# Optimization experiments

Measured on AMD Instinct MI355X. Metric: run time of the kernel, lower is better.

Reference implementation:

```python
import jax, jax.numpy as jnp
import numpy as np

EMBED_DIM = 256
NUM_HEADS = 4
HEAD_DIM = EMBED_DIM // NUM_HEADS
B, N0, N1 = 4, 2048, 2048


def setup_inputs() -> dict:
    key = jax.random.key(0)
    ks = jax.random.split(key, 16)
    d = EMBED_DIM
    s = 0.02
    return {
        "x0": jax.random.normal(ks[0], (B, N0, d), jnp.float32),
        "x1": jax.random.normal(ks[1], (B, N1, d), jnp.float32),
        "Wqk": jax.random.normal(ks[2], (d, d), jnp.float32) * s,
        "bqk": jnp.zeros((d,), jnp.float32),
        "Wv": jax.random.normal(ks[3], (d, d), jnp.float32) * s,
        "bv": jnp.zeros((d,), jnp.float32),
        "Wout": jax.random.normal(ks[4], (d, d), jnp.float32) * s,
        "bout": jnp.zeros((d,), jnp.float32),
        "W0": jax.random.normal(ks[5], (2 * d, 2 * d), jnp.float32) * s,
        "b0": jnp.zeros((2 * d,), jnp.float32),
        "ln_scale": jnp.ones((2 * d,), jnp.float32),
        "ln_bias": jnp.zeros((2 * d,), jnp.float32),
        "W3": jax.random.normal(ks[6], (2 * d, d), jnp.float32) * s,
        "b3": jnp.zeros((d,), jnp.float32),
    }


def _heads(t, b, n):
    # [b, n, d] -> [b, h, n, hd]
    return t.reshape(b, n, NUM_HEADS, HEAD_DIM).transpose(0, 2, 1, 3)


def _layernorm(y, scale, bias, eps=1e-5):
    mu = jnp.mean(y, axis=-1, keepdims=True)
    var = jnp.mean(jnp.square(y - mu), axis=-1, keepdims=True)
    return (y - mu) * jax.lax.rsqrt(var + eps) * scale + bias


def reference(x0, x1, Wqk, bqk, Wv, bv, Wout, bout, W0, b0, ln_scale, ln_bias, W3, b3):
    b, n0, d = x0.shape
    _, n1, _ = x1.shape
    scale = 1.0 / jnp.sqrt(jnp.float32(HEAD_DIM))

    qk0 = _heads(x0 @ Wqk + bqk, b, n0)
    qk1 = _heads(x1 @ Wqk + bqk, b, n1)
    v0 = _heads(x0 @ Wv + bv, b, n0)
    v1 = _heads(x1 @ Wv + bv, b, n1)

    # shared logits: [b, h, n0, n1]
    logits01 = jnp.einsum('bhid,bhjd->bhij', qk0, qk1) * scale
    attn01 = jax.nn.softmax(logits01, axis=-1)
    m0 = jnp.einsum('bhij,bhjd->bhid', attn01, v1)
    attn10 = jax.nn.softmax(logits01.transpose(0, 1, 3, 2), axis=-1)
    m1 = jnp.einsum('bhji,bhjd->bhid', attn10.transpose(0, 1, 3, 2), v0)

    m0 = m0.transpose(0, 2, 1, 3).reshape(b, n0, d) @ Wout + bout
    m1 = m1.transpose(0, 2, 1, 3).reshape(b, n1, d) @ Wout + bout

    def ffn(x, m):
        y = jnp.concatenate([x, m], axis=-1) @ W0 + b0
        y = _layernorm(y, ln_scale, ln_bias)
        y = jax.nn.gelu(y, approximate=False)
        return x + y @ W3 + b3

    return ffn(x0, m0), ffn(x1, m1)
```

## Files before the change

### kernel.cpp

```cpp
#include <hip/hip_runtime.h>
#include <math.h>

#define BATCH 4
#define SEQ 2048
#define DMODEL 256
#define NH 4
#define HD 64
#define MROWS (BATCH * SEQ)

typedef short bf16x8 __attribute__((ext_vector_type(8)));
typedef float f32x4 __attribute__((ext_vector_type(4)));

__device__ __forceinline__ unsigned short f2bf(float x) {
  union { float f; unsigned int u; } v;
  v.f = x;
  unsigned int r = (v.u + 0x7FFF + ((v.u >> 16) & 1)) >> 16;
  return (unsigned short)r;
}
__device__ __forceinline__ unsigned short f2bf_trunc(float x) {
  union { float f; unsigned int u; } v;
  v.f = x;
  return (unsigned short)(v.u >> 16);
}
__device__ __forceinline__ float bf2f(unsigned short u) {
  union { unsigned int u; float f; } v;
  v.u = ((unsigned int)u) << 16;
  return v.f;
}

__global__ __launch_bounds__(256) void cast_x(
    const float* __restrict__ x0, const float* __restrict__ x1,
    unsigned short* __restrict__ x0b, unsigned short* __restrict__ x1b) {
  const int n4 = (MROWS * DMODEL) / 4;
  for (int i = blockIdx.x * 256 + threadIdx.x; i < 2 * n4; i += gridDim.x * 256) {
    const float* src = (i < n4) ? x0 : x1;
    unsigned short* dst = (i < n4) ? x0b : x1b;
    int j = (i < n4) ? i : i - n4;
    float4 v = *(const float4*)&src[j * 4];
    ushort4 o = {f2bf(v.x), f2bf(v.y), f2bf(v.z), f2bf(v.w)};
    *(ushort4*)&dst[j * 4] = o;
  }
}

__global__ __launch_bounds__(256) void cast_w(
    const float* __restrict__ Wqk, const float* __restrict__ Wv,
    const float* __restrict__ Wout, const float* __restrict__ W0,
    const float* __restrict__ W3,
    unsigned short* __restrict__ Wqkt, unsigned short* __restrict__ Wvt,
    unsigned short* __restrict__ Woutt, unsigned short* __restrict__ W0t,
    unsigned short* __restrict__ W3t) {
  int gid = blockIdx.x * 256 + threadIdx.x;
  const float* src; unsigned short* dst; int K, N, idx;
  if (gid < 65536)        { src = Wqk;  dst = Wqkt;  K = 256; N = 256; idx = gid; }
  else if (gid < 131072)  { src = Wv;   dst = Wvt;   K = 256; N = 256; idx = gid - 65536; }
  else if (gid < 196608)  { src = Wout; dst = Woutt; K = 256; N = 256; idx = gid - 131072; }
  else if (gid < 458752)  { src = W0;   dst = W0t;   K = 512; N = 512; idx = gid - 196608; }
  else if (gid < 589824)  { src = W3;   dst = W3t;   K = 512; N = 256; idx = gid - 458752; }
  else return;
  int k = idx / N, n = idx % N;
  dst[n * K + k] = f2bf(src[idx]);
}

template <int MODE>
__global__ __launch_bounds__(256) void gemm2(
    const unsigned short* __restrict__ A_0, const unsigned short* __restrict__ A_1,
    const unsigned short* __restrict__ A2_0, const unsigned short* __restrict__ A2_1,
    const unsigned short* __restrict__ Wt, const float* __restrict__ bias,
    const float* __restrict__ resid_0, const float* __restrict__ resid_1,
    void* __restrict__ C_0, void* __restrict__ C_1, int N, int K) {
  __shared__ unsigned short lds[12288];

  const int t = threadIdx.x;
  const int w = t >> 6, lane = t & 63;
  const int qd = lane >> 4, l15 = lane & 15;
  const int row0 = blockIdx.x * 128;
  const int col0 = blockIdx.y * 64;
  const int z = blockIdx.z;
  const unsigned short* A  = z ? A_1 : A_0;
  const unsigned short* A2 = z ? A2_1 : A2_0;
  const float* resid = z ? resid_1 : resid_0;
  void* Cv = z ? C_1 : C_0;

  f32x4 acc[2][4];
#pragma unroll
  for (int mh = 0; mh < 2; ++mh)
#pragma unroll
    for (int tn = 0; tn < 4; ++tn) acc[mh][tn] = (f32x4){0.f, 0.f, 0.f, 0.f};

  for (int k0 = 0; k0 < K; k0 += 64) {
    __syncthreads();
#pragma unroll
    for (int pp = 0; pp < 6; ++pp) {
      int g = pp * 4 + w;
      uint4 d;
      if (g < 16) {
        int tm = g >> 1, s = g & 1;
        const unsigned short* Ap = A;
        int kk = k0 + s * 32 + qd * 8, lda = K;
        if (MODE == 2) {
          Ap = (k0 < 256) ? A : A2;
          kk = (k0 & 255) + s * 32 + qd * 8;
          lda = 256;
        }
        d = *(const uint4*)&Ap[(size_t)(row0 + tm * 16 + l15) * lda + kk];
        *(uint4*)&lds[(g * 64 + lane) * 8] = d;
      } else {
        int tn = (g - 16) >> 1, s = g & 1;
        d = *(const uint4*)&Wt[(size_t)(col0 + tn * 16 + l15) * K + k0 + s * 32 + qd * 8];
        *(uint4*)&lds[8192 + (((tn * 2 + s) * 64 + lane)) * 8] = d;
      }
    }
    __syncthreads();

    bf16x8 aA[2][2];
#pragma unroll
    for (int mh = 0; mh < 2; ++mh)
#pragma unroll
      for (int s = 0; s < 2; ++s)
        aA[mh][s] = *(const bf16x8*)&lds[((((w * 2 + mh) * 2 + s)) * 64 + lane) * 8];
#pragma unroll
    for (int tn = 0; tn < 4; ++tn) {
      bf16x8 b0 = *(const bf16x8*)&lds[8192 + ((tn * 2 + 0) * 64 + lane) * 8];
      bf16x8 b1 = *(const bf16x8*)&lds[8192 + ((tn * 2 + 1) * 64 + lane) * 8];
#pragma unroll
      for (int mh = 0; mh < 2; ++mh) {
        acc[mh][tn] = __builtin_amdgcn_mfma_f32_16x16x32_bf16(aA[mh][0], b0, acc[mh][tn], 0, 0, 0);
        acc[mh][tn] = __builtin_amdgcn_mfma_f32_16x16x32_bf16(aA[mh][1], b1, acc[mh][tn], 0, 0, 0);
      }
    }
  }

  if (MODE == 1) {
    __syncthreads();
#pragma unroll
    for (int tn = 0; tn < 4; ++tn) {
      int col = col0 + tn * 16 + l15;
      float bb = bias[col];
#pragma unroll
      for (int mh = 0; mh < 2; ++mh)
#pragma unroll
        for (int r = 0; r < 4; ++r) {
          int rloc = w * 32 + mh * 16 + qd * 4 + r;
          lds[(tn * 16 + l15) * 130 + rloc] = f2bf(acc[mh][tn][r] + bb);
        }
    }
    __syncthreads();
    unsigned short* Vt = (unsigned short*)Cv;
    int b_ = row0 >> 11;
    int h_ = blockIdx.y;
    int seq0 = row0 & 2047;
    for (int c = t; c < 1024; c += 256) {
      int dloc = c >> 4, sc = c & 15;
      uint4 d = *(const uint4*)&lds[dloc * 130 + sc * 8];
      *(uint4*)&Vt[((size_t)(b_ * NH + h_) * HD + dloc) * SEQ + seq0 + sc * 8] = d;
    }
    return;
  }

#pragma unroll
  for (int tn = 0; tn < 4; ++tn) {
    int col = col0 + tn * 16 + l15;
    float bb = bias[col];
#pragma unroll
    for (int mh = 0; mh < 2; ++mh)
#pragma unroll
      for (int r = 0; r < 4; ++r) {
        size_t grow = row0 + w * 32 + mh * 16 + qd * 4 + r;
        float v = acc[mh][tn][r] + bb;
        if (MODE == 3) {
          ((float*)Cv)[grow * N + col] = resid[grow * N + col] + v;
        } else {
          ((unsigned short*)Cv)[grow * N + col] = f2bf(v);
        }
      }
  }
}

__global__ __launch_bounds__(256) void flash_v4(
    const unsigned short* __restrict__ qk0, const unsigned short* __restrict__ qk1,
    const unsigned short* __restrict__ vt0, const unsigned short* __restrict__ vt1,
    unsigned short* __restrict__ m0, unsigned short* __restrict__ m1) {
  __shared__ unsigned short lds[8192];

  const int t = threadIdx.x;
  const int w = t >> 6, lane = t & 63;
  const int qd = lane >> 4, l15 = lane & 15;
  const int qt = blockIdx.x, h = blockIdx.y, z = blockIdx.z;
  const int dir = z & 1, b = z >> 1;
  const unsigned short* Qb = dir ? qk1 : qk0;
  const unsigned short* Kb = dir ? qk0 : qk1;
  const unsigned short* Vt = dir ? vt0 : vt1;
  unsigned short* Ob = dir ? m1 : m0;

  const size_t qrow0 = (size_t)b * SEQ + (size_t)qt * 128;
  const int hoff = h * HD;
  const unsigned short* vtb = Vt + (size_t)(b * NH + h) * HD * SEQ;
  const float sc2 = 0.125f * 1.44269504f;

  bf16x8 qf[2][2];
#pragma unroll
  for (int qh = 0; qh < 2; ++qh)
#pragma unroll
    for (int s = 0; s < 2; ++s)
      qf[qh][s] = *(const bf16x8*)&Qb[(qrow0 + w * 32 + qh * 16 + l15) * DMODEL + hoff + s * 32 + qd * 8];

  f32x4 Oacc[2][4];
#pragma unroll
  for (int qh = 0; qh < 2; ++qh)
#pragma unroll
    for (int td = 0; td < 4; ++td) Oacc[qh][td] = (f32x4){0.f, 0.f, 0.f, 0.f};
  float l_lane[2] = {0.f, 0.f};

  for (int kt = 0; kt < SEQ / 64; ++kt) {
    const size_t kbase = (size_t)b * SEQ + (size_t)kt * 64;
    __syncthreads();
#pragma unroll
    for (int pp = 0; pp < 4; ++pp) {
      int g = pp * 4 + w;
      uint4 d;
      if (g < 8) {
        int tk = g >> 1, s = g & 1;
        int kvl = (tk >> 1) * 32 + (l15 >> 2) * 8 + (tk & 1) * 4 + (l15 & 3);
        d = *(const uint4*)&Kb[(kbase + kvl) * DMODEL + hoff + s * 32 + qd * 8];
      } else {
        int td = (g - 8) >> 1, s = g & 1;
        d = *(const uint4*)&vtb[(size_t)(td * 16 + l15) * SEQ + kt * 64 + s * 32 + qd * 8];
      }
      *(uint4*)&lds[(g * 64 + lane) * 8] = d;
    }
    __syncthreads();

    bf16x8 kf[4][2], vf[4][2];
#pragma unroll
    for (int tk = 0; tk < 4; ++tk)
#pragma unroll
      for (int s = 0; s < 2; ++s) {
        kf[tk][s] = *(const bf16x8*)&lds[((tk * 2 + s) * 64 + lane) * 8];
        vf[tk][s] = *(const bf16x8*)&lds[4096 + ((tk * 2 + s) * 64 + lane) * 8];
      }

#pragma unroll
    for (int qh = 0; qh < 2; ++qh) {
      f32x4 S[4];
#pragma unroll
      for (int tk = 0; tk < 4; ++tk) {
        f32x4 a = {0.f, 0.f, 0.f, 0.f};
        a = __builtin_amdgcn_mfma_f32_16x16x32_bf16(kf[tk][0], qf[qh][0], a, 0, 0, 0);
        a = __builtin_amdgcn_mfma_f32_16x16x32_bf16(kf[tk][1], qf[qh][1], a, 0, 0, 0);
        S[tk] = a;
      }
      float p[4][4];
      float rs = 0.f;
#pragma unroll
      for (int tk = 0; tk < 4; ++tk)
#pragma unroll
        for (int r = 0; r < 4; ++r) {
          float pv = exp2f(S[tk][r] * sc2);
          p[tk][r] = pv;
          rs += pv;
        }
      l_lane[qh] += rs;
      bf16x8 pA[2];
#pragma unroll
      for (int s = 0; s < 2; ++s) {
        bf16x8 v;
#pragma unroll
        for (int j = 0; j < 4; ++j) {
          v[j] = (short)f2bf_trunc(p[2 * s][j]);
          v[j + 4] = (short)f2bf_trunc(p[2 * s + 1][j]);
        }
        pA[s] = v;
      }
#pragma unroll
      for (int td = 0; td < 4; ++td) {
        Oacc[qh][td] = __builtin_amdgcn_mfma_f32_16x16x32_bf16(pA[0], vf[td][0], Oacc[qh][td], 0, 0, 0);
        Oacc[qh][td] = __builtin_amdgcn_mfma_f32_16x16x32_bf16(pA[1], vf[td][1], Oacc[qh][td], 0, 0, 0);
      }
    }
  }

#pragma unroll
  for (int qh = 0; qh < 2; ++qh) {
    float l = l_lane[qh];
    l += __shfl_xor(l, 16);
    l += __shfl_xor(l, 32);
    float linv = 1.0f / l;
#pragma unroll
    for (int r = 0; r < 4; ++r) {
      float lq = __shfl(linv, qd * 20 + r, 64);
      size_t row = qrow0 + w * 32 + qh * 16 + qd * 4 + r;
#pragma unroll
      for (int td = 0; td < 4; ++td)
        Ob[row * DMODEL + hoff + td * 16 + l15] = f2bf(Oacc[qh][td][r] * lq);
    }
  }
}

__global__ __launch_bounds__(256) void ln_gelu2(
    unsigned short* __restrict__ Y0, unsigned short* __restrict__ Y1,
    const float* __restrict__ sc, const float* __restrict__ bi) {
  const int t = threadIdx.x;
  const int row = blockIdx.x & (MROWS - 1);
  unsigned short* Y = (blockIdx.x >> 13) ? Y1 : Y0;
  unsigned short* p = Y + (size_t)row * 512;
  unsigned int u = *(const unsigned int*)&p[t * 2];
  float v0 = bf2f((unsigned short)(u & 0xFFFF));
  float v1 = bf2f((unsigned short)(u >> 16));
  float s1 = v0 + v1, s2 = v0 * v0 + v1 * v1;
#pragma unroll
  for (int m = 1; m < 64; m <<= 1) {
    s1 += __shfl_xor(s1, m);
    s2 += __shfl_xor(s2, m);
  }
  __shared__ float red[8];
  int w = t >> 6;
  if ((t & 63) == 0) { red[w] = s1; red[4 + w] = s2; }
  __syncthreads();
  s1 = red[0] + red[1] + red[2] + red[3];
  s2 = red[4] + red[5] + red[6] + red[7];
  float mu = s1 * (1.0f / 512.0f);
  float var = s2 * (1.0f / 512.0f) - mu * mu;
  float rstd = rsqrtf(var + 1e-5f);
  float y0 = (v0 - mu) * rstd * sc[t * 2] + bi[t * 2];
  float y1 = (v1 - mu) * rstd * sc[t * 2 + 1] + bi[t * 2 + 1];
  y0 = 0.5f * y0 * (1.0f + erff(y0 * 0.70710678118654752f));
  y1 = 0.5f * y1 * (1.0f + erff(y1 * 0.70710678118654752f));
  unsigned int o = (unsigned int)f2bf(y0) | ((unsigned int)f2bf(y1) << 16);
  *(unsigned int*)&p[t * 2] = o;
}

extern "C" void kernel_launch(void* const* d_in, const int* in_sizes, int n_in,
                              void* d_out, int out_size, void* d_ws,
                              size_t ws_size, hipStream_t stream) {
  const float* x0   = (const float*)d_in[0];
  const float* x1   = (const float*)d_in[1];
  const float* Wqk  = (const float*)d_in[2];
  const float* bqk  = (const float*)d_in[3];
  const float* Wv   = (const float*)d_in[4];
  const float* bv   = (const float*)d_in[5];
  const float* Wout = (const float*)d_in[6];
  const float* bout = (const float*)d_in[7];
  const float* W0   = (const float*)d_in[8];
  const float* b0   = (const float*)d_in[9];
  const float* lns  = (const float*)d_in[10];
  const float* lnb  = (const float*)d_in[11];
  const float* W3   = (const float*)d_in[12];
  const float* b3   = (const float*)d_in[13];

  char* ws = (char*)d_ws;
  const size_t MB = 1024 * 1024;
  unsigned short* x0b   = (unsigned short*)(ws + 0 * MB);
  unsigned short* x1b   = (unsigned short*)(ws + 4 * MB);
  unsigned short* Wqkt  = (unsigned short*)(ws + 8 * MB);
  unsigned short* Wvt   = (unsigned short*)(ws + 9 * MB);
  unsigned short* Woutt = (unsigned short*)(ws + 10 * MB);
  unsigned short* W0t   = (unsigned short*)(ws + 11 * MB);
  unsigned short* W3t   = (unsigned short*)(ws + 12 * MB);
  unsigned short* qk0b  = (unsigned short*)(ws + 13 * MB);
  unsigned short* qk1b  = (unsigned short*)(ws + 17 * MB);
  unsigned short* vt0   = (unsigned short*)(ws + 21 * MB);
  unsigned short* vt1   = (unsigned short*)(ws + 25 * MB);
  unsigned short* m0b   = (unsigned short*)(ws + 29 * MB);
  unsigned short* m1b   = (unsigned short*)(ws + 33 * MB);
  unsigned short* mp0b  = (unsigned short*)(ws + 37 * MB);
  unsigned short* mp1b  = (unsigned short*)(ws + 41 * MB);
  unsigned short* y0b   = (unsigned short*)(ws + 13 * MB);
  unsigned short* y1b   = (unsigned short*)(ws + 21 * MB);
  float* out0 = (float*)d_out;
  float* out1 = out0 + (size_t)MROWS * DMODEL;

  dim3 blk(256);
  dim3 gP(MROWS / 128, 4, 2);
  dim3 gF1(MROWS / 128, 8, 2);
  dim3 gA(SEQ / 128, NH, BATCH * 2);

  cast_x<<<dim3(4096), blk, 0, stream>>>(x0, x1, x0b, x1b);
  cast_w<<<dim3(589824 / 256), blk, 0, stream>>>(Wqk, Wv, Wout, W0, W3,
                                                 Wqkt, Wvt, Woutt, W0t, W3t);

  gemm2<0><<<gP, blk, 0, stream>>>(x0b, x1b, nullptr, nullptr, Wqkt, bqk,
                                   nullptr, nullptr, qk0b, qk1b, DMODEL, DMODEL);
  gemm2<1><<<gP, blk, 0, stream>>>(x0b, x1b, nullptr, nullptr, Wvt, bv,
                                   nullptr, nullptr, vt0, vt1, DMODEL, DMODEL);

  flash_v4<<<gA, blk, 0, stream>>>(qk0b, qk1b, vt0, vt1, m0b, m1b);

  gemm2<0><<<gP, blk, 0, stream>>>(m0b, m1b, nullptr, nullptr, Woutt, bout,
                                   nullptr, nullptr, mp0b, mp1b, DMODEL, DMODEL);

  gemm2<2><<<gF1, blk, 0, stream>>>(x0b, x1b, mp0b, mp1b, W0t, b0,
                                    nullptr, nullptr, y0b, y1b, 512, 512);

  ln_gelu2<<<dim3(2 * MROWS), blk, 0, stream>>>(y0b, y1b, lns, lnb);

  gemm2<3><<<gP, blk, 0, stream>>>(y0b, y1b, nullptr, nullptr, W3t, b3,
                                   x0, x1, out0, out1, DMODEL, 512);
}
```

Measured before the change: 274.8 us.

## Fold Wout into W0, fuse QK/V projection, split-K flash attention with DMA loads

Precomputes Wout·W0[256:] and the matching bias so the output-projection GEMM disappears. The QK and V projections become one GEMM with a concatenated weight, and the softmax scale is folded into the stored QK values. Flash attention is split into two halves over the keys, which doubles the grid; a combine kernel merges the partial outputs and row sums. All GEMM and flash tile loads now use global_load_lds DMA, the GEMM tile shrinks to 64 rows, and LN-GELU processes one row per wave. In exchange it adds fp32 partial-output traffic and a combine pass, and the QK scale is applied to bf16-rounded values before the dot product.

```diff
diff --git a/kernel.cpp b/kernel.cpp
--- a/kernel.cpp
+++ b/kernel.cpp
@@ -6,196 +6,241 @@
 #define DMODEL 256
 #define NH 4
 #define HD 64
-#define MROWS (BATCH * SEQ)
+#define MROWS 8192
+#define QKSCALE 0.4246608905f
 
 typedef short bf16x8 __attribute__((ext_vector_type(8)));
 typedef float f32x4 __attribute__((ext_vector_type(4)));
-
-__device__ __forceinline__ unsigned short f2bf(float x) {
+typedef unsigned short us;
+
+__device__ __forceinline__ us f2bf(float x) {
   union { float f; unsigned int u; } v;
   v.f = x;
   unsigned int r = (v.u + 0x7FFF + ((v.u >> 16) & 1)) >> 16;
-  return (unsigned short)r;
-}
-__device__ __forceinline__ unsigned short f2bf_trunc(float x) {
+  return (us)r;
+}
+__device__ __forceinline__ us f2bf_trunc(float x) {
   union { float f; unsigned int u; } v;
   v.f = x;
-  return (unsigned short)(v.u >> 16);
-}
-__device__ __forceinline__ float bf2f(unsigned short u) {
+  return (us)(v.u >> 16);
+}
+__device__ __forceinline__ float bf2f(us u) {
   union { unsigned int u; float f; } v;
   v.u = ((unsigned int)u) << 16;
   return v.f;
 }
+__device__ __forceinline__ void dma16(const void* g, void* l) {
+  auto gp = (const __attribute__((address_space(1))) unsigned int*)(unsigned long long)(uintptr_t)g;
+  auto lp = (__attribute__((address_space(3))) unsigned int*)(unsigned int)(uintptr_t)l;
+  __builtin_amdgcn_global_load_lds(gp, lp, 16, 0, 0);
+}
 
 __global__ __launch_bounds__(256) void cast_x(
     const float* __restrict__ x0, const float* __restrict__ x1,
-    unsigned short* __restrict__ x0b, unsigned short* __restrict__ x1b) {
+    us* __restrict__ x0b, us* __restrict__ x1b) {
   const int n4 = (MROWS * DMODEL) / 4;
-  for (int i = blockIdx.x * 256 + threadIdx.x; i < 2 * n4; i += gridDim.x * 256) {
-    const float* src = (i < n4) ? x0 : x1;
-    unsigned short* dst = (i < n4) ? x0b : x1b;
-    int j = (i < n4) ? i : i - n4;
-    float4 v = *(const float4*)&src[j * 4];
-    ushort4 o = {f2bf(v.x), f2bf(v.y), f2bf(v.z), f2bf(v.w)};
-    *(ushort4*)&dst[j * 4] = o;
-  }
+  int i = blockIdx.x * 256 + threadIdx.x;
+  const float* src = (i < n4) ? x0 : x1;
+  us* dst = (i < n4) ? x0b : x1b;
+  int j = (i < n4) ? i : i - n4;
+  float4 v = *(const float4*)&src[j * 4];
+  ushort4 o = {f2bf(v.x), f2bf(v.y), f2bf(v.z), f2bf(v.w)};
+  *(ushort4*)&dst[j * 4] = o;
 }
 
 __global__ __launch_bounds__(256) void cast_w(
     const float* __restrict__ Wqk, const float* __restrict__ Wv,
+    const float* __restrict__ W0, const float* __restrict__ W3,
+    const float* __restrict__ bqk, const float* __restrict__ bv,
+    us* __restrict__ Wqvt, us* __restrict__ W1t, us* __restrict__ W3t,
+    float* __restrict__ bias_qv) {
+  int gid = blockIdx.x * 256 + threadIdx.x;
+  if (gid < 65536) {
+    int k = gid >> 8, j = gid & 255;
+    Wqvt[j * 256 + k] = f2bf(Wqk[gid]);
+  } else if (gid < 131072) {
+    int i = gid - 65536;
+    int k = i >> 8, j = i & 255;
+    Wqvt[(256 + j) * 256 + k] = f2bf(Wv[i]);
+  } else if (gid < 262144) {
+    int i = gid - 131072;
+    int k = i >> 9, j = i & 511;
+    W1t[j * 512 + k] = f2bf(W0[i]);
+  } else if (gid < 393216) {
+    int i = gid - 262144;
+    int k = i >> 8, j = i & 255;
+    W3t[j * 512 + k] = f2bf(W3[i]);
+  } else if (gid < 393728) {
+    int j = gid - 393216;
+    bias_qv[j] = (j < 256) ? bqk[j] : bv[j - 256];
+  }
+}
+
+__global__ __launch_bounds__(256) void wcomb_k(
     const float* __restrict__ Wout, const float* __restrict__ W0,
-    const float* __restrict__ W3,
-    unsigned short* __restrict__ Wqkt, unsigned short* __restrict__ Wvt,
-    unsigned short* __restrict__ Woutt, unsigned short* __restrict__ W0t,
-    unsigned short* __restrict__ W3t) {
-  int gid = blockIdx.x * 256 + threadIdx.x;
-  const float* src; unsigned short* dst; int K, N, idx;
-  if (gid < 65536)        { src = Wqk;  dst = Wqkt;  K = 256; N = 256; idx = gid; }
-  else if (gid < 131072)  { src = Wv;   dst = Wvt;   K = 256; N = 256; idx = gid - 65536; }
-  else if (gid < 196608)  { src = Wout; dst = Woutt; K = 256; N = 256; idx = gid - 131072; }
-  else if (gid < 458752)  { src = W0;   dst = W0t;   K = 512; N = 512; idx = gid - 196608; }
-  else if (gid < 589824)  { src = W3;   dst = W3t;   K = 512; N = 256; idx = gid - 458752; }
-  else return;
-  int k = idx / N, n = idx % N;
-  dst[n * K + k] = f2bf(src[idx]);
+    const float* __restrict__ b0, const float* __restrict__ bout,
+    us* __restrict__ W1t, float* __restrict__ bias1) {
+  int t = threadIdx.x, i = blockIdx.x;
+  if (i < 256) {
+    float a0 = 0.f, a1 = 0.f;
+    for (int k = 0; k < 256; ++k) {
+      float wk = Wout[i * 256 + k];
+      const float* row = &W0[(256 + k) * 512];
+      a0 += wk * row[t];
+      a1 += wk * row[t + 256];
+    }
+    W1t[t * 512 + 256 + i] = f2bf(a0);
+    W1t[(t + 256) * 512 + 256 + i] = f2bf(a1);
+  } else {
+    float a0 = b0[t], a1 = b0[t + 256];
+    for (int k = 0; k < 256; ++k) {
+      float bk = bout[k];
+      const float* row = &W0[(256 + k) * 512];
+      a0 += bk * row[t];
+      a1 += bk * row[t + 256];
+    }
+    bias1[t] = a0;
+    bias1[t + 256] = a1;
+  }
 }
 
 template <int MODE>
-__global__ __launch_bounds__(256) void gemm2(
-    const unsigned short* __restrict__ A_0, const unsigned short* __restrict__ A_1,
-    const unsigned short* __restrict__ A2_0, const unsigned short* __restrict__ A2_1,
-    const unsigned short* __restrict__ Wt, const float* __restrict__ bias,
-    const float* __restrict__ resid_0, const float* __restrict__ resid_1,
-    void* __restrict__ C_0, void* __restrict__ C_1, int N, int K) {
-  __shared__ unsigned short lds[12288];
-
-  const int t = threadIdx.x;
-  const int w = t >> 6, lane = t & 63;
+__global__ __launch_bounds__(256) void gemm3(
+    const us* __restrict__ A0, const us* __restrict__ A1,
+    const us* __restrict__ Am0, const us* __restrict__ Am1,
+    const us* __restrict__ Wt, const float* __restrict__ bias,
+    const float* __restrict__ r0_, const float* __restrict__ r1_,
+    void* __restrict__ C0_, void* __restrict__ C1_,
+    void* __restrict__ V0_, void* __restrict__ V1_, int K) {
+  __shared__ us lds[8192];
+  const int t = threadIdx.x, w = t >> 6, lane = t & 63;
   const int qd = lane >> 4, l15 = lane & 15;
-  const int row0 = blockIdx.x * 128;
-  const int col0 = blockIdx.y * 64;
+  const int row0 = blockIdx.x * 64;
+  const int coltile = blockIdx.y, col0 = coltile * 64;
   const int z = blockIdx.z;
-  const unsigned short* A  = z ? A_1 : A_0;
-  const unsigned short* A2 = z ? A2_1 : A2_0;
-  const float* resid = z ? resid_1 : resid_0;
-  void* Cv = z ? C_1 : C_0;
-
-  f32x4 acc[2][4];
-#pragma unroll
-  for (int mh = 0; mh < 2; ++mh)
-#pragma unroll
-    for (int tn = 0; tn < 4; ++tn) acc[mh][tn] = (f32x4){0.f, 0.f, 0.f, 0.f};
+  const us* Ax = z ? A1 : A0;
+  const us* Am = z ? Am1 : Am0;
+
+  f32x4 acc[4];
+#pragma unroll
+  for (int tn = 0; tn < 4; ++tn) acc[tn] = (f32x4){0.f, 0.f, 0.f, 0.f};
 
   for (int k0 = 0; k0 < K; k0 += 64) {
     __syncthreads();
 #pragma unroll
-    for (int pp = 0; pp < 6; ++pp) {
+    for (int pp = 0; pp < 4; ++pp) {
       int g = pp * 4 + w;
-      uint4 d;
-      if (g < 16) {
+      const us* src;
+      if (g < 8) {
         int tm = g >> 1, s = g & 1;
-        const unsigned short* Ap = A;
-        int kk = k0 + s * 32 + qd * 8, lda = K;
-        if (MODE == 2) {
-          Ap = (k0 < 256) ? A : A2;
-          kk = (k0 & 255) + s * 32 + qd * 8;
+        const us* Ap = Ax;
+        int kk = k0 + s * 32 + qd * 8;
+        int lda = K;
+        if (MODE == 1) {
+          Ap = (k0 < 256) ? Ax : Am;
+          kk = kk & 255;
           lda = 256;
         }
-        d = *(const uint4*)&Ap[(size_t)(row0 + tm * 16 + l15) * lda + kk];
-        *(uint4*)&lds[(g * 64 + lane) * 8] = d;
+        src = &Ap[(size_t)(row0 + tm * 16 + l15) * lda + kk];
       } else {
-        int tn = (g - 16) >> 1, s = g & 1;
-        d = *(const uint4*)&Wt[(size_t)(col0 + tn * 16 + l15) * K + k0 + s * 32 + qd * 8];
-        *(uint4*)&lds[8192 + (((tn * 2 + s) * 64 + lane)) * 8] = d;
-      }
+        int tn = (g - 8) >> 1, s = g & 1;
+        src = &Wt[(size_t)(col0 + tn * 16 + l15) * K + k0 + s * 32 + qd * 8];
+      }
+      dma16(src, &lds[g * 512]);
     }
     __syncthreads();
 
-    bf16x8 aA[2][2];
-#pragma unroll
-    for (int mh = 0; mh < 2; ++mh)
-#pragma unroll
-      for (int s = 0; s < 2; ++s)
-        aA[mh][s] = *(const bf16x8*)&lds[((((w * 2 + mh) * 2 + s)) * 64 + lane) * 8];
+    bf16x8 aA0 = *(const bf16x8*)&lds[((w * 2 + 0) * 64 + lane) * 8];
+    bf16x8 aA1 = *(const bf16x8*)&lds[((w * 2 + 1) * 64 + lane) * 8];
 #pragma unroll
     for (int tn = 0; tn < 4; ++tn) {
-      bf16x8 b0 = *(const bf16x8*)&lds[8192 + ((tn * 2 + 0) * 64 + lane) * 8];
-      bf16x8 b1 = *(const bf16x8*)&lds[8192 + ((tn * 2 + 1) * 64 + lane) * 8];
-#pragma unroll
-      for (int mh = 0; mh < 2; ++mh) {
-        acc[mh][tn] = __builtin_amdgcn_mfma_f32_16x16x32_bf16(aA[mh][0], b0, acc[mh][tn], 0, 0, 0);
-        acc[mh][tn] = __builtin_amdgcn_mfma_f32_16x16x32_bf16(aA[mh][1], b1, acc[mh][tn], 0, 0, 0);
-      }
-    }
-  }
-
-  if (MODE == 1) {
-    __syncthreads();
+      bf16x8 b0v = *(const bf16x8*)&lds[((8 + tn * 2 + 0) * 64 + lane) * 8];
+      bf16x8 b1v = *(const bf16x8*)&lds[((8 + tn * 2 + 1) * 64 + lane) * 8];
+      acc[tn] = __builtin_amdgcn_mfma_f32_16x16x32_bf16(aA0, b0v, acc[tn], 0, 0, 0);
+      acc[tn] = __builtin_amdgcn_mfma_f32_16x16x32_bf16(aA1, b1v, acc[tn], 0, 0, 0);
+    }
+  }
+
+  if (MODE == 0) {
+    if (coltile < 4) {
+      us* C = (us*)(z ? C1_ : C0_);
+#pragma unroll
+      for (int tn = 0; tn < 4; ++tn) {
+        int col = col0 + tn * 16 + l15;
+        float bb = bias[col];
+#pragma unroll
+        for (int r = 0; r < 4; ++r) {
+          size_t grow = row0 + w * 16 + qd * 4 + r;
+          C[grow * 256 + col] = f2bf((acc[tn][r] + bb) * QKSCALE);
+        }
+      }
+    } else {
+      __syncthreads();
+      int h_ = coltile - 4;
+#pragma unroll
+      for (int tn = 0; tn < 4; ++tn) {
+        int col = col0 + tn * 16 + l15;
+        float bb = bias[col];
+#pragma unroll
+        for (int r = 0; r < 4; ++r) {
+          int rloc = w * 16 + qd * 4 + r;
+          lds[(tn * 16 + l15) * 66 + rloc] = f2bf(acc[tn][r] + bb);
+        }
+      }
+      __syncthreads();
+      us* Vt = (us*)(z ? V1_ : V0_);
+      int b_ = row0 >> 11, seq0 = row0 & 2047;
+      for (int c = t; c < 512; c += 256) {
+        int dloc = c >> 3, scc = c & 7;
+        uint4 d = *(const uint4*)&lds[dloc * 66 + scc * 8];
+        *(uint4*)&Vt[((size_t)(b_ * NH + h_) * HD + dloc) * SEQ + seq0 + scc * 8] = d;
+      }
+    }
+  } else if (MODE == 1) {
+    us* C = (us*)(z ? C1_ : C0_);
 #pragma unroll
     for (int tn = 0; tn < 4; ++tn) {
       int col = col0 + tn * 16 + l15;
       float bb = bias[col];
 #pragma unroll
-      for (int mh = 0; mh < 2; ++mh)
-#pragma unroll
-        for (int r = 0; r < 4; ++r) {
-          int rloc = w * 32 + mh * 16 + qd * 4 + r;
-          lds[(tn * 16 + l15) * 130 + rloc] = f2bf(acc[mh][tn][r] + bb);
-        }
-    }
-    __syncthreads();
-    unsigned short* Vt = (unsigned short*)Cv;
-    int b_ = row0 >> 11;
-    int h_ = blockIdx.y;
-    int seq0 = row0 & 2047;
-    for (int c = t; c < 1024; c += 256) {
-      int dloc = c >> 4, sc = c & 15;
-      uint4 d = *(const uint4*)&lds[dloc * 130 + sc * 8];
-      *(uint4*)&Vt[((size_t)(b_ * NH + h_) * HD + dloc) * SEQ + seq0 + sc * 8] = d;
-    }
-    return;
-  }
-
-#pragma unroll
-  for (int tn = 0; tn < 4; ++tn) {
-    int col = col0 + tn * 16 + l15;
-    float bb = bias[col];
-#pragma unroll
-    for (int mh = 0; mh < 2; ++mh)
-#pragma unroll
       for (int r = 0; r < 4; ++r) {
-        size_t grow = row0 + w * 32 + mh * 16 + qd * 4 + r;
-        float v = acc[mh][tn][r] + bb;
-        if (MODE == 3) {
-          ((float*)Cv)[grow * N + col] = resid[grow * N + col] + v;
-        } else {
-          ((unsigned short*)Cv)[grow * N + col] = f2bf(v);
-        }
-      }
-  }
-}
-
-__global__ __launch_bounds__(256) void flash_v4(
-    const unsigned short* __restrict__ qk0, const unsigned short* __restrict__ qk1,
-    const unsigned short* __restrict__ vt0, const unsigned short* __restrict__ vt1,
-    unsigned short* __restrict__ m0, unsigned short* __restrict__ m1) {
-  __shared__ unsigned short lds[8192];
-
-  const int t = threadIdx.x;
-  const int w = t >> 6, lane = t & 63;
+        size_t grow = row0 + w * 16 + qd * 4 + r;
+        C[grow * 512 + col] = f2bf(acc[tn][r] + bb);
+      }
+    }
+  } else {
+    float* C = (float*)(z ? C1_ : C0_);
+    const float* R = z ? r1_ : r0_;
+#pragma unroll
+    for (int tn = 0; tn < 4; ++tn) {
+      int col = col0 + tn * 16 + l15;
+      float bb = bias[col];
+#pragma unroll
+      for (int r = 0; r < 4; ++r) {
+        size_t grow = row0 + w * 16 + qd * 4 + r;
+        C[grow * 256 + col] = R[grow * 256 + col] + acc[tn][r] + bb;
+      }
+    }
+  }
+}
+
+__global__ __launch_bounds__(256) void flash_v5(
+    const us* __restrict__ qk0, const us* __restrict__ qk1,
+    const us* __restrict__ vt0, const us* __restrict__ vt1,
+    float* __restrict__ Opart, float* __restrict__ lpart) {
+  __shared__ us lds[8192];
+  const int t = threadIdx.x, w = t >> 6, lane = t & 63;
   const int qd = lane >> 4, l15 = lane & 15;
-  const int qt = blockIdx.x, h = blockIdx.y, z = blockIdx.z;
-  const int dir = z & 1, b = z >> 1;
-  const unsigned short* Qb = dir ? qk1 : qk0;
-  const unsigned short* Kb = dir ? qk0 : qk1;
-  const unsigned short* Vt = dir ? vt0 : vt1;
-  unsigned short* Ob = dir ? m1 : m0;
-
+  const int qt = blockIdx.x & 15, half = blockIdx.x >> 4;
+  const int h = blockIdx.y, z = blockIdx.z, dir = z & 1, b = z >> 1;
+  const us* Qb = dir ? qk1 : qk0;
+  const us* Kb = dir ? qk0 : qk1;
+  const us* Vt = dir ? vt0 : vt1;
+  float* Op = Opart + (size_t)(dir * 2 + half) * (MROWS * DMODEL);
+  float* lp = lpart + ((size_t)(dir * 2 + half) * NH + h) * MROWS;
   const size_t qrow0 = (size_t)b * SEQ + (size_t)qt * 128;
   const int hoff = h * HD;
-  const unsigned short* vtb = Vt + (size_t)(b * NH + h) * HD * SEQ;
-  const float sc2 = 0.125f * 1.44269504f;
+  const us* vtb = Vt + (size_t)(b * NH + h) * HD * SEQ;
 
   bf16x8 qf[2][2];
 #pragma unroll
@@ -211,22 +256,22 @@
     for (int td = 0; td < 4; ++td) Oacc[qh][td] = (f32x4){0.f, 0.f, 0.f, 0.f};
   float l_lane[2] = {0.f, 0.f};
 
-  for (int kt = 0; kt < SEQ / 64; ++kt) {
+  for (int kt = half * 16; kt < half * 16 + 16; ++kt) {
     const size_t kbase = (size_t)b * SEQ + (size_t)kt * 64;
     __syncthreads();
 #pragma unroll
     for (int pp = 0; pp < 4; ++pp) {
       int g = pp * 4 + w;
-      uint4 d;
+      const us* src;
       if (g < 8) {
         int tk = g >> 1, s = g & 1;
         int kvl = (tk >> 1) * 32 + (l15 >> 2) * 8 + (tk & 1) * 4 + (l15 & 3);
-        d = *(const uint4*)&Kb[(kbase + kvl) * DMODEL + hoff + s * 32 + qd * 8];
+        src = &Kb[(kbase + kvl) * DMODEL + hoff + s * 32 + qd * 8];
       } else {
         int td = (g - 8) >> 1, s = g & 1;
-        d = *(const uint4*)&vtb[(size_t)(td * 16 + l15) * SEQ + kt * 64 + s * 32 + qd * 8];
-      }
-      *(uint4*)&lds[(g * 64 + lane) * 8] = d;
+        src = &vtb[(size_t)(td * 16 + l15) * SEQ + kt * 64 + s * 32 + qd * 8];
+      }
+      dma16(src, &lds[g * 512]);
     }
     __syncthreads();
 
@@ -236,7 +281,7 @@
 #pragma unroll
       for (int s = 0; s < 2; ++s) {
         kf[tk][s] = *(const bf16x8*)&lds[((tk * 2 + s) * 64 + lane) * 8];
-        vf[tk][s] = *(const bf16x8*)&lds[4096 + ((tk * 2 + s) * 64 + lane) * 8];
+        vf[tk][s] = *(const bf16x8*)&lds[((8 + tk * 2 + s) * 64 + lane) * 8];
       }
 
 #pragma unroll
@@ -255,7 +300,7 @@
       for (int tk = 0; tk < 4; ++tk)
 #pragma unroll
         for (int r = 0; r < 4; ++r) {
-          float pv = exp2f(S[tk][r] * sc2);
+          float pv = exp2f(S[tk][r]);
           p[tk][r] = pv;
           rs += pv;
         }
@@ -284,49 +329,82 @@
     float l = l_lane[qh];
     l += __shfl_xor(l, 16);
     l += __shfl_xor(l, 32);
-    float linv = 1.0f / l;
+    if (qd == 0) lp[qrow0 + w * 32 + qh * 16 + l15] = l;
 #pragma unroll
     for (int r = 0; r < 4; ++r) {
-      float lq = __shfl(linv, qd * 20 + r, 64);
       size_t row = qrow0 + w * 32 + qh * 16 + qd * 4 + r;
 #pragma unroll
       for (int td = 0; td < 4; ++td)
-        Ob[row * DMODEL + hoff + td * 16 + l15] = f2bf(Oacc[qh][td][r] * lq);
-    }
-  }
-}
-
-__global__ __launch_bounds__(256) void ln_gelu2(
-    unsigned short* __restrict__ Y0, unsigned short* __restrict__ Y1,
+        Op[row * DMODEL + hoff + td * 16 + l15] = Oacc[qh][td][r];
+    }
+  }
+}
+
+__global__ __launch_bounds__(256) void combine_k(
+    const float* __restrict__ Opart, const float* __restrict__ lpart,
+    us* __restrict__ m0b, us* __restrict__ m1b) {
+  int gid = blockIdx.x * 256 + threadIdx.x;
+  int dir = gid >= (MROWS * DMODEL / 4);
+  int idx = gid - dir * (MROWS * DMODEL / 4);
+  int row = idx >> 6;
+  int c4 = (idx & 63) << 2;
+  int h = c4 >> 6;
+  const float* Oa = Opart + (size_t)(dir * 2 + 0) * (MROWS * DMODEL);
+  const float* Ob = Opart + (size_t)(dir * 2 + 1) * (MROWS * DMODEL);
+  float la = lpart[((size_t)(dir * 2 + 0) * NH + h) * MROWS + row];
+  float lb = lpart[((size_t)(dir * 2 + 1) * NH + h) * MROWS + row];
+  float inv = 1.0f / (la + lb);
+  float4 a = *(const float4*)&Oa[(size_t)row * DMODEL + c4];
+  float4 bv = *(const float4*)&Ob[(size_t)row * DMODEL + c4];
+  us* m = dir ? m1b : m0b;
+  ushort4 o = {f2bf((a.x + bv.x) * inv), f2bf((a.y + bv.y) * inv),
+               f2bf((a.z + bv.z) * inv), f2bf((a.w + bv.w) * inv)};
+  *(ushort4*)&m[(size_t)row * DMODEL + c4] = o;
+}
+
+__global__ __launch_bounds__(256) void ln_gelu3(
+    us* __restrict__ Y0, us* __restrict__ Y1,
     const float* __restrict__ sc, const float* __restrict__ bi) {
-  const int t = threadIdx.x;
-  const int row = blockIdx.x & (MROWS - 1);
-  unsigned short* Y = (blockIdx.x >> 13) ? Y1 : Y0;
-  unsigned short* p = Y + (size_t)row * 512;
-  unsigned int u = *(const unsigned int*)&p[t * 2];
-  float v0 = bf2f((unsigned short)(u & 0xFFFF));
-  float v1 = bf2f((unsigned short)(u >> 16));
-  float s1 = v0 + v1, s2 = v0 * v0 + v1 * v1;
+  int w = threadIdx.x >> 6, lane = threadIdx.x & 63;
+  int ridx = blockIdx.x * 4 + w;
+  us* Y = (ridx >= MROWS) ? Y1 : Y0;
+  int row = ridx & (MROWS - 1);
+  us* p = Y + (size_t)row * 512 + lane * 8;
+  uint4 u = *(const uint4*)p;
+  unsigned int uu[4] = {u.x, u.y, u.z, u.w};
+  float v[8];
+#pragma unroll
+  for (int i = 0; i < 4; ++i) {
+    v[2 * i] = bf2f((us)(uu[i] & 0xFFFF));
+    v[2 * i + 1] = bf2f((us)(uu[i] >> 16));
+  }
+  float s1 = 0.f, s2 = 0.f;
+#pragma unroll
+  for (int i = 0; i < 8; ++i) { s1 += v[i]; s2 += v[i] * v[i]; }
 #pragma unroll
   for (int m = 1; m < 64; m <<= 1) {
     s1 += __shfl_xor(s1, m);
     s2 += __shfl_xor(s2, m);
   }
-  __shared__ float red[8];
-  int w = t >> 6;
-  if ((t & 63) == 0) { red[w] = s1; red[4 + w] = s2; }
-  __syncthreads();
-  s1 = red[0] + red[1] + red[2] + red[3];
-  s2 = red[4] + red[5] + red[6] + red[7];
   float mu = s1 * (1.0f / 512.0f);
   float var = s2 * (1.0f / 512.0f) - mu * mu;
   float rstd = rsqrtf(var + 1e-5f);
-  float y0 = (v0 - mu) * rstd * sc[t * 2] + bi[t * 2];
-  float y1 = (v1 - mu) * rstd * sc[t * 2 + 1] + bi[t * 2 + 1];
-  y0 = 0.5f * y0 * (1.0f + erff(y0 * 0.70710678118654752f));
-  y1 = 0.5f * y1 * (1.0f + erff(y1 * 0.70710678118654752f));
-  unsigned int o = (unsigned int)f2bf(y0) | ((unsigned int)f2bf(y1) << 16);
-  *(unsigned int*)&p[t * 2] = o;
+  int c0 = lane * 8;
+  float4 scA = *(const float4*)&sc[c0], scB = *(const float4*)&sc[c0 + 4];
+  float4 biA = *(const float4*)&bi[c0], biB = *(const float4*)&bi[c0 + 4];
+  float scv[8] = {scA.x, scA.y, scA.z, scA.w, scB.x, scB.y, scB.z, scB.w};
+  float biv[8] = {biA.x, biA.y, biA.z, biA.w, biB.x, biB.y, biB.z, biB.w};
+  unsigned int ou[4];
+#pragma unroll
+  for (int i = 0; i < 4; ++i) {
+    float y0 = (v[2 * i] - mu) * rstd * scv[2 * i] + biv[2 * i];
+    float y1 = (v[2 * i + 1] - mu) * rstd * scv[2 * i + 1] + biv[2 * i + 1];
+    y0 = 0.5f * y0 * (1.0f + erff(y0 * 0.70710678118654752f));
+    y1 = 0.5f * y1 * (1.0f + erff(y1 * 0.70710678118654752f));
+    ou[i] = (unsigned int)f2bf(y0) | ((unsigned int)f2bf(y1) << 16);
+  }
+  uint4 o = {ou[0], ou[1], ou[2], ou[3]};
+  *(uint4*)p = o;
 }
 
 extern "C" void kernel_launch(void* const* d_in, const int* in_sizes, int n_in,
@@ -349,50 +427,47 @@
 
   char* ws = (char*)d_ws;
   const size_t MB = 1024 * 1024;
-  unsigned short* x0b   = (unsigned short*)(ws + 0 * MB);
-  unsigned short* x1b   = (unsigned short*)(ws + 4 * MB);
-  unsigned short* Wqkt  = (unsigned short*)(ws + 8 * MB);
-  unsigned short* Wvt   = (unsigned short*)(ws + 9 * MB);
-  unsigned short* Woutt = (unsigned short*)(ws + 10 * MB);
-  unsigned short* W0t   = (unsigned short*)(ws + 11 * MB);
-  unsigned short* W3t   = (unsigned short*)(ws + 12 * MB);
-  unsigned short* qk0b  = (unsigned short*)(ws + 13 * MB);
-  unsigned short* qk1b  = (unsigned short*)(ws + 17 * MB);
-  unsigned short* vt0   = (unsigned short*)(ws + 21 * MB);
-  unsigned short* vt1   = (unsigned short*)(ws + 25 * MB);
-  unsigned short* m0b   = (unsigned short*)(ws + 29 * MB);
-  unsigned short* m1b   = (unsigned short*)(ws + 33 * MB);
-  unsigned short* mp0b  = (unsigned short*)(ws + 37 * MB);
-  unsigned short* mp1b  = (unsigned short*)(ws + 41 * MB);
-  unsigned short* y0b   = (unsigned short*)(ws + 13 * MB);
-  unsigned short* y1b   = (unsigned short*)(ws + 21 * MB);
+  us* x0b  = (us*)(ws + 0 * MB);
+  us* x1b  = (us*)(ws + 4 * MB);
+  us* Wqvt = (us*)(ws + 8 * MB);
+  us* W1t  = (us*)(ws + 8 * MB + 262144);
+  us* W3t  = (us*)(ws + 8 * MB + 786432);
+  float* bias_qv = (float*)(ws + 9 * MB);
+  float* bias1   = (float*)(ws + 9 * MB + 4096);
+  us* qk0b = (us*)(ws + 10 * MB);
+  us* qk1b = (us*)(ws + 14 * MB);
+  us* vt0  = (us*)(ws + 18 * MB);
+  us* vt1  = (us*)(ws + 22 * MB);
+  us* m0b  = (us*)(ws + 26 * MB);
+  us* m1b  = (us*)(ws + 30 * MB);
+  us* y0b  = (us*)(ws + 10 * MB);
+  us* y1b  = (us*)(ws + 18 * MB);
+  float* Opart = (float*)(ws + 34 * MB);
+  float* lpart = (float*)(ws + 66 * MB);
   float* out0 = (float*)d_out;
   float* out1 = out0 + (size_t)MROWS * DMODEL;
 
   dim3 blk(256);
-  dim3 gP(MROWS / 128, 4, 2);
-  dim3 gF1(MROWS / 128, 8, 2);
-  dim3 gA(SEQ / 128, NH, BATCH * 2);
 
   cast_x<<<dim3(4096), blk, 0, stream>>>(x0, x1, x0b, x1b);
-  cast_w<<<dim3(589824 / 256), blk, 0, stream>>>(Wqk, Wv, Wout, W0, W3,
-                                                 Wqkt, Wvt, Woutt, W0t, W3t);
-
-  gemm2<0><<<gP, blk, 0, stream>>>(x0b, x1b, nullptr, nullptr, Wqkt, bqk,
-                                   nullptr, nullptr, qk0b, qk1b, DMODEL, DMODEL);
-  gemm2<1><<<gP, blk, 0, stream>>>(x0b, x1b, nullptr, nullptr, Wvt, bv,
-                                   nullptr, nullptr, vt0, vt1, DMODEL, DMODEL);
-
-  flash_v4<<<gA, blk, 0, stream>>>(qk0b, qk1b, vt0, vt1, m0b, m1b);
-
-  gemm2<0><<<gP, blk, 0, stream>>>(m0b, m1b, nullptr, nullptr, Woutt, bout,
-                                   nullptr, nullptr, mp0b, mp1b, DMODEL, DMODEL);
-
-  gemm2<2><<<gF1, blk, 0, stream>>>(x0b, x1b, mp0b, mp1b, W0t, b0,
-                                    nullptr, nullptr, y0b, y1b, 512, 512);
-
-  ln_gelu2<<<dim3(2 * MROWS), blk, 0, stream>>>(y0b, y1b, lns, lnb);
-
-  gemm2<3><<<gP, blk, 0, stream>>>(y0b, y1b, nullptr, nullptr, W3t, b3,
-                                   x0, x1, out0, out1, DMODEL, 512);
-}
+  cast_w<<<dim3(1538), blk, 0, stream>>>(Wqk, Wv, W0, W3, bqk, bv,
+                                         Wqvt, W1t, W3t, bias_qv);
+  wcomb_k<<<dim3(257), blk, 0, stream>>>(Wout, W0, b0, bout, W1t, bias1);
+
+  gemm3<0><<<dim3(128, 8, 2), blk, 0, stream>>>(
+      x0b, x1b, nullptr, nullptr, Wqvt, bias_qv, nullptr, nullptr,
+      qk0b, qk1b, vt0, vt1, 256);
+
+  flash_v5<<<dim3(32, 4, 8), blk, 0, stream>>>(qk0b, qk1b, vt0, vt1, Opart, lpart);
+  combine_k<<<dim3(4096), blk, 0, stream>>>(Opart, lpart, m0b, m1b);
+
+  gemm3<1><<<dim3(128, 8, 2), blk, 0, stream>>>(
+      x0b, x1b, m0b, m1b, W1t, bias1, nullptr, nullptr,
+      y0b, y1b, nullptr, nullptr, 512);
+
+  ln_gelu3<<<dim3(4096), blk, 0, stream>>>(y0b, y1b, lns, lnb);
+
+  gemm3<2><<<dim3(128, 4, 2), blk, 0, stream>>>(
+      y0b, y1b, nullptr, nullptr, W3t, b3, x0, x1,
+      out0, out1, nullptr, nullptr, 512);
+}
```

New measurement: 268.5 us. 2.3% less time.
